# Kernel tuning notes

Hardware: AMD Instinct MI355X
Metric: run time of the kernel (lower is better)

The kernel has to match this reference:

```python
import jax, jax.numpy as jnp
import numpy as np

_EPS = 1e-06


def setup_inputs() -> dict:
    key = jax.random.key(0)
    k1, k2, k3, k4, k5 = jax.random.split(key, 5)
    B, N = 2, 8192
    return {
        "kp_before": jax.random.normal(k1, (B, N, 3), dtype=jnp.float32),
        "kp_warped_pred": jax.random.normal(k2, (B, N, 3), dtype=jnp.float32),
        "pose_gt": jax.random.normal(k3, (B, 3, 4), dtype=jnp.float32),
        "overlap_weights": jax.random.uniform(k4, (B, N), dtype=jnp.float32),
        "inlier_logits": jax.random.normal(k5, (B, N), dtype=jnp.float32),
    }


def _bce_with_logits(x, z):
    # elementwise BCEWithLogits: z*softplus(-x) + (1-z)*softplus(x)
    return z * jax.nn.softplus(-x) + (1.0 - z) * jax.nn.softplus(x)


def _balanced_loss(logits, label):
    # BalancedLoss: mean BCE within each of the 2 label groups, averaged over groups
    bce = _bce_with_logits(logits, label)
    loss = jnp.float32(0.0)
    for i in range(2):
        mask = (label == i).astype(jnp.float32)
        cnt = jnp.sum(mask)
        group = jnp.where(cnt > 0, jnp.sum(bce * mask) / jnp.maximum(cnt, 1.0), 0.0)
        loss = loss + group / 2.0
    return loss


def reference(kp_before, kp_warped_pred, pose_gt, overlap_weights, inlier_logits):
    B, N, _ = kp_before.shape
    M = B * N
    # se3_transform_list: warped_gt[b] = kp_before[b] @ R[b]^T + t[b]
    R = pose_gt[:, :, :3]            # [B,3,3]
    t = pose_gt[:, :, 3]             # [B,3]
    kp_warped_gt = jnp.einsum('bij,bnj->bni', R, kp_before) + t[:, None, :]
    # torch.cat(list, dim=0) over equal-sized chunks == reshape
    pred = kp_warped_pred.reshape(M, 3)
    gt = kp_warped_gt.reshape(M, 3)
    corr_err = pred - gt               # [M,3]
    # pairwise L2 distance matrix [M,M] (O(N^2) traffic) + 1-NN argmin
    sq = (jnp.sum(pred * pred, axis=1)[:, None]
          + jnp.sum(gt * gt, axis=1)[None, :]
          - 2.0 * (pred @ gt.T))
    dist_map = jnp.sqrt(jnp.maximum(sq, 0.0))
    knn_ind = jnp.argmin(dist_map, axis=1)
    binary_mask = (knn_ind == jnp.arange(M)).astype(jnp.float32)
    inlier_err = _balanced_loss(inlier_logits.reshape(M), binary_mask)
    # metric == 'mae'
    err = jnp.sum(jnp.abs(corr_err), axis=-1)  # [M]
    w = overlap_weights.reshape(M)
    mean_err = jnp.sum(w * err) / jnp.maximum(jnp.sum(w), _EPS)
    return mean_err + inlier_err
```

## Files before the change

### kernel.cpp

```cpp
#include <hip/hip_runtime.h>
#include <cstdint>

#define TPB 256
#define IT 8
#define JCHUNK 64

__global__ void prep_kernel(const float* __restrict__ kp_before,
                            const float* __restrict__ pred,
                            const float* __restrict__ pose,
                            float4* __restrict__ gt4,
                            float* __restrict__ thr,
                            unsigned int* __restrict__ good,
                            float* __restrict__ accum,
                            int M, int N) {
    int tid = blockIdx.x * blockDim.x + threadIdx.x;
    if (tid < 8) accum[tid] = 0.0f;
    int stride = gridDim.x * blockDim.x;
    for (int i = tid; i < M; i += stride) {
        good[i] = 0u;
        int b = i / N;
        const float* P = pose + b * 12;
        float k0 = kp_before[3*i+0];
        float k1 = kp_before[3*i+1];
        float k2 = kp_before[3*i+2];
        float g0 = fmaf(P[2],  k2, fmaf(P[1], k1, P[0]*k0)) + P[3];
        float g1 = fmaf(P[6],  k2, fmaf(P[5], k1, P[4]*k0)) + P[7];
        float g2 = fmaf(P[10], k2, fmaf(P[9], k1, P[8]*k0)) + P[11];
        float sg;
        {
            #pragma clang fp contract(off)
            sg = (g0*g0 + g1*g1) + g2*g2;
        }
        gt4[i] = make_float4(g0, g1, g2, sg);

        float p0 = pred[3*i+0], p1 = pred[3*i+1], p2 = pred[3*i+2];
        float sp;
        {
            #pragma clang fp contract(off)
            sp = (p0*p0 + p1*p1) + p2*p2;
        }
        float t0 = 2.0f*p0, t1 = 2.0f*p1, t2 = 2.0f*p2;
        float dot2 = fmaf(t2, g2, fmaf(t1, g1, t0*g0));
        float v = (sp + sg) - dot2;
        thr[i] = fmaxf(v, 0.0f);
    }
}

__global__ void __launch_bounds__(TPB, 8) flags_kernel(
        const float* __restrict__ pred,
        const float4* __restrict__ gt4,
        const float* __restrict__ thr,
        unsigned int* __restrict__ good,
        int M, int numI) {
    __shared__ float4 sh[JCHUNK];
    int ic = blockIdx.x % numI;
    int jc = blockIdx.x / numI;
    int j0 = jc * JCHUNK;
    int jmax = M - j0; if (jmax > JCHUNK) jmax = JCHUNK;

    for (int k = threadIdx.x; k < jmax; k += TPB) {
        sh[k] = gt4[j0 + k];
    }
    __syncthreads();

    float tp0[IT], tp1[IT], tp2[IT], sp[IT], m[IT];
    int ibase = ic * (TPB * IT) + threadIdx.x;
    #pragma unroll
    for (int k = 0; k < IT; k++) {
        int i = ibase + k * TPB;
        if (i >= M) i = M - 1;
        float p0 = pred[3*i+0], p1 = pred[3*i+1], p2 = pred[3*i+2];
        {
            #pragma clang fp contract(off)
            sp[k] = (p0*p0 + p1*p1) + p2*p2;
        }
        tp0[k] = 2.0f * p0;
        tp1[k] = 2.0f * p1;
        tp2[k] = 2.0f * p2;
        m[k] = __uint_as_float(0x7f7fffffu);
    }

    int j = 0;
    for (; j + 1 < jmax; j += 2) {
        float4 ga = sh[j];
        float4 gb = sh[j + 1];
        #pragma unroll
        for (int k = 0; k < IT; k++) {
            float va = (sp[k] + ga.w) -
                       fmaf(tp2[k], ga.z, fmaf(tp1[k], ga.y, tp0[k] * ga.x));
            float vb = (sp[k] + gb.w) -
                       fmaf(tp2[k], gb.z, fmaf(tp1[k], gb.y, tp0[k] * gb.x));
            m[k] = fminf(fminf(va, vb), m[k]);
        }
    }
    if (j < jmax) {
        float4 ga = sh[j];
        #pragma unroll
        for (int k = 0; k < IT; k++) {
            float va = (sp[k] + ga.w) -
                       fmaf(tp2[k], ga.z, fmaf(tp1[k], ga.y, tp0[k] * ga.x));
            m[k] = fminf(va, m[k]);
        }
    }

    int j1 = j0 + jmax;
    #pragma unroll
    for (int k = 0; k < IT; k++) {
        int i = ibase + k * TPB;
        if (i >= M) continue;
        float dii = thr[i];
        float vminc = fmaxf(m[k], 0.0f);
        bool bad;
        if (i >= j1) {
            bad = (vminc <= dii);
        } else {
            bad = (vminc < dii);
            if (!bad && i > j0) {
                int je = i < j1 ? (i - j0) : jmax;
                for (int jj = 0; jj < je; jj++) {
                    float4 g = sh[jj];
                    float v = (sp[k] + g.w) -
                              fmaf(tp2[k], g.z, fmaf(tp1[k], g.y, tp0[k] * g.x));
                    if (fmaxf(v, 0.0f) <= dii) { bad = true; break; }
                }
            }
        }
        if (!bad) atomicAdd(&good[i], 1u);
    }
}

__device__ inline float wave_red(float v) {
    #pragma unroll
    for (int off = 32; off > 0; off >>= 1) v += __shfl_down(v, off, 64);
    return v;
}

__global__ void finalize_kernel(const float* __restrict__ pred,
                                const float4* __restrict__ gt4,
                                const float* __restrict__ ow,
                                const float* __restrict__ logits,
                                const unsigned int* __restrict__ good,
                                float* __restrict__ accum, int M, int numJ) {
    float werr = 0.f, wsum = 0.f, b1 = 0.f, c1 = 0.f, b0 = 0.f, c0 = 0.f;
    int stride = gridDim.x * blockDim.x;
    for (int i = blockIdx.x * blockDim.x + threadIdx.x; i < M; i += stride) {
        float x = logits[i];
        float l1p = log1pf(expf(-fabsf(x)));
        if (good[i] == (unsigned int)numJ) {
            b1 += fmaxf(-x, 0.f) + l1p; c1 += 1.f;
        } else {
            b0 += fmaxf(x, 0.f) + l1p;  c0 += 1.f;
        }
        float4 g = gt4[i];
        float p0 = pred[3*i+0], p1 = pred[3*i+1], p2 = pred[3*i+2];
        float e = (fabsf(p0 - g.x) + fabsf(p1 - g.y)) + fabsf(p2 - g.z);
        float wi = ow[i];
        werr += wi * e;
        wsum += wi;
    }
    werr = wave_red(werr); wsum = wave_red(wsum);
    b1 = wave_red(b1); c1 = wave_red(c1);
    b0 = wave_red(b0); c0 = wave_red(c0);
    if ((threadIdx.x & 63) == 0) {
        atomicAdd(&accum[0], werr);
        atomicAdd(&accum[1], wsum);
        atomicAdd(&accum[2], b1);
        atomicAdd(&accum[3], c1);
        atomicAdd(&accum[4], b0);
        atomicAdd(&accum[5], c0);
    }
}

__global__ void scalar_kernel(const float* __restrict__ accum,
                              float* __restrict__ out) {
    float mean_err = accum[0] / fmaxf(accum[1], 1e-6f);
    float g1 = (accum[3] > 0.f) ? (accum[2] / fmaxf(accum[3], 1.f)) : 0.f;
    float g0 = (accum[5] > 0.f) ? (accum[4] / fmaxf(accum[5], 1.f)) : 0.f;
    out[0] = mean_err + (g0 * 0.5f + g1 * 0.5f);
}

extern "C" void kernel_launch(void* const* d_in, const int* in_sizes, int n_in,
                              void* d_out, int out_size, void* d_ws, size_t ws_size,
                              hipStream_t stream) {
    const float* kp_before = (const float*)d_in[0];
    const float* pred      = (const float*)d_in[1];
    const float* pose      = (const float*)d_in[2];
    const float* ow        = (const float*)d_in[3];
    const float* logits    = (const float*)d_in[4];
    float* out = (float*)d_out;

    int M = in_sizes[3];
    int B = in_sizes[2] / 12;
    int N = M / B;

    char* ws = (char*)d_ws;
    float4* gt4 = (float4*)ws;
    float* thr = (float*)(ws + (size_t)M * 16);
    unsigned int* good = (unsigned int*)(ws + (size_t)M * 20);
    float* accum = (float*)(ws + (size_t)M * 24);

    int prep_blocks = (M + TPB - 1) / TPB;
    hipLaunchKernelGGL(prep_kernel, dim3(prep_blocks), dim3(TPB), 0, stream,
                       kp_before, pred, pose, gt4, thr, good, accum, M, N);

    int numI = (M + TPB * IT - 1) / (TPB * IT);
    int numJ = (M + JCHUNK - 1) / JCHUNK;
    hipLaunchKernelGGL(flags_kernel, dim3(numI * numJ), dim3(TPB), 0, stream,
                       pred, gt4, thr, good, M, numI);

    hipLaunchKernelGGL(finalize_kernel, dim3(64), dim3(TPB), 0, stream,
                       pred, gt4, ow, logits, good, accum, M, numJ);

    hipLaunchKernelGGL(scalar_kernel, dim3(1), dim3(1), 0, stream,
                       accum, out);
}
```

Measured before the change: 121.3 us.

## Replace tiled all-pairs min with per-row wavefront scan and early exit

After: 155.6 us. 28.3% more time.

```diff
diff --git a/kernel.cpp b/kernel.cpp
--- a/kernel.cpp
+++ b/kernel.cpp
@@ -2,8 +2,6 @@
 #include <cstdint>
 
 #define TPB 256
-#define IT 8
-#define JCHUNK 64
 
 __global__ void prep_kernel(const float* __restrict__ kp_before,
                             const float* __restrict__ pred,
@@ -46,87 +44,52 @@
     }
 }
 
-__global__ void __launch_bounds__(TPB, 8) flags_kernel(
+#define SCAN_U 4
+
+__global__ void __launch_bounds__(TPB) scan_kernel(
         const float* __restrict__ pred,
         const float4* __restrict__ gt4,
         const float* __restrict__ thr,
         unsigned int* __restrict__ good,
-        int M, int numI) {
-    __shared__ float4 sh[JCHUNK];
-    int ic = blockIdx.x % numI;
-    int jc = blockIdx.x / numI;
-    int j0 = jc * JCHUNK;
-    int jmax = M - j0; if (jmax > JCHUNK) jmax = JCHUNK;
+        int M) {
+    int wid  = (blockIdx.x * blockDim.x + threadIdx.x) >> 6;
+    int lane = threadIdx.x & 63;
+    if (wid >= M) return;
+    int i = __builtin_amdgcn_readfirstlane(wid);
 
-    for (int k = threadIdx.x; k < jmax; k += TPB) {
-        sh[k] = gt4[j0 + k];
+    float p0 = pred[3*i+0], p1 = pred[3*i+1], p2 = pred[3*i+2];
+    float sp;
+    {
+        #pragma clang fp contract(off)
+        sp = (p0*p0 + p1*p1) + p2*p2;
     }
-    __syncthreads();
+    float tp0 = 2.0f*p0, tp1 = 2.0f*p1, tp2 = 2.0f*p2;
+    float dii = thr[i];
 
-    float tp0[IT], tp1[IT], tp2[IT], sp[IT], m[IT];
-    int ibase = ic * (TPB * IT) + threadIdx.x;
-    #pragma unroll
-    for (int k = 0; k < IT; k++) {
-        int i = ibase + k * TPB;
-        if (i >= M) i = M - 1;
-        float p0 = pred[3*i+0], p1 = pred[3*i+1], p2 = pred[3*i+2];
-        {
-            #pragma clang fp contract(off)
-            sp[k] = (p0*p0 + p1*p1) + p2*p2;
+    bool bad = false;
+    for (int jb = 0; jb < M; jb += 64 * SCAN_U) {
+        int j0 = jb + lane;
+        float4 g[SCAN_U];
+        int    jj[SCAN_U];
+        #pragma unroll
+        for (int u = 0; u < SCAN_U; u++) {
+            int j = j0 + 64 * u;
+            if (j > M - 1) j = M - 1;
+            jj[u] = j;
+            g[u] = gt4[j];
         }
-        tp0[k] = 2.0f * p0;
-        tp1[k] = 2.0f * p1;
-        tp2[k] = 2.0f * p2;
-        m[k] = __uint_as_float(0x7f7fffffu);
+        bool h = false;
+        #pragma unroll
+        for (int u = 0; u < SCAN_U; u++) {
+            float v = (sp + g[u].w) -
+                      fmaf(tp2, g[u].z, fmaf(tp1, g[u].y, tp0 * g[u].x));
+            float c = fmaxf(v, 0.0f);
+            int j = jj[u];
+            h = h || (c < dii && j != i) || (c == dii && j < i);
+        }
+        if (__any(h)) { bad = true; break; }
     }
-
-    int j = 0;
-    for (; j + 1 < jmax; j += 2) {
-        float4 ga = sh[j];
-        float4 gb = sh[j + 1];
-        #pragma unroll
-        for (int k = 0; k < IT; k++) {
-            float va = (sp[k] + ga.w) -
-                       fmaf(tp2[k], ga.z, fmaf(tp1[k], ga.y, tp0[k] * ga.x));
-            float vb = (sp[k] + gb.w) -
-                       fmaf(tp2[k], gb.z, fmaf(tp1[k], gb.y, tp0[k] * gb.x));
-            m[k] = fminf(fminf(va, vb), m[k]);
-        }
-    }
-    if (j < jmax) {
-        float4 ga = sh[j];
-        #pragma unroll
-        for (int k = 0; k < IT; k++) {
-            float va = (sp[k] + ga.w) -
-                       fmaf(tp2[k], ga.z, fmaf(tp1[k], ga.y, tp0[k] * ga.x));
-            m[k] = fminf(va, m[k]);
-        }
-    }
-
-    int j1 = j0 + jmax;
-    #pragma unroll
-    for (int k = 0; k < IT; k++) {
-        int i = ibase + k * TPB;
-        if (i >= M) continue;
-        float dii = thr[i];
-        float vminc = fmaxf(m[k], 0.0f);
-        bool bad;
-        if (i >= j1) {
-            bad = (vminc <= dii);
-        } else {
-            bad = (vminc < dii);
-            if (!bad && i > j0) {
-                int je = i < j1 ? (i - j0) : jmax;
-                for (int jj = 0; jj < je; jj++) {
-                    float4 g = sh[jj];
-                    float v = (sp[k] + g.w) -
-                              fmaf(tp2[k], g.z, fmaf(tp1[k], g.y, tp0[k] * g.x));
-                    if (fmaxf(v, 0.0f) <= dii) { bad = true; break; }
-                }
-            }
-        }
-        if (!bad) atomicAdd(&good[i], 1u);
-    }
+    if (lane == 0) good[i] = bad ? 0u : 1u;
 }
 
 __device__ inline float wave_red(float v) {
@@ -203,13 +166,12 @@
     hipLaunchKernelGGL(prep_kernel, dim3(prep_blocks), dim3(TPB), 0, stream,
                        kp_before, pred, pose, gt4, thr, good, accum, M, N);
 
-    int numI = (M + TPB * IT - 1) / (TPB * IT);
-    int numJ = (M + JCHUNK - 1) / JCHUNK;
-    hipLaunchKernelGGL(flags_kernel, dim3(numI * numJ), dim3(TPB), 0, stream,
-                       pred, gt4, thr, good, M, numI);
+    int scan_blocks = (M * 64 + TPB - 1) / TPB;
+    hipLaunchKernelGGL(scan_kernel, dim3(scan_blocks), dim3(TPB), 0, stream,
+                       pred, gt4, thr, good, M);
 
     hipLaunchKernelGGL(finalize_kernel, dim3(64), dim3(TPB), 0, stream,
-                       pred, gt4, ow, logits, good, accum, M, numJ);
+                       pred, gt4, ow, logits, good, accum, M, 1);
 
     hipLaunchKernelGGL(scalar_kernel, dim3(1), dim3(1), 0, stream,
                        accum, out);
```
